# Performance work log

Measured on AMD Instinct MI355X. Metric: run time of the kernel, lower is better.

Reference implementation:

```python
import jax, jax.numpy as jnp
import numpy as np

TEMPERATURE = 0.07
EPS = 1e-8  # torch CosineSimilarity norm clamp

N, D, NUM_CLASSES = 4096, 768, 128


def setup_inputs() -> dict:
    key = jax.random.key(0)
    k1, k2, k3 = jax.random.split(key, 3)
    img_emb = jax.random.normal(k1, (N, D), dtype=jnp.float32)
    text_emb = jax.random.normal(k2, (N, D), dtype=jnp.float32)
    labels = jax.random.randint(k3, (N,), 0, NUM_CLASSES, dtype=jnp.int64)
    return {"img_emb": img_emb, "text_emb": text_emb, "labels": labels}


def reference(img_emb, text_emb, labels):
    # cosine similarity via normalize + matmul (avoids O(N^2 D) broadcast)
    img_n = img_emb / jnp.maximum(jnp.linalg.norm(img_emb, axis=-1, keepdims=True), EPS)
    txt_n = text_emb / jnp.maximum(jnp.linalg.norm(text_emb, axis=-1, keepdims=True), EPS)
    logits = jnp.einsum('id,jd->ij', img_n, txt_n) / TEMPERATURE  # [N, N]

    pos_mask = (labels[:, None] == labels[None, :]).astype(logits.dtype)  # [N, N]

    img2text = -(pos_mask * jax.nn.log_softmax(logits, axis=1)).sum(1).mean()
    text2img = -(pos_mask * jax.nn.log_softmax(logits, axis=0)).sum(0).mean()
    return (img2text + text2img) / 2
```

## Files before the change

kernel.cpp:

```cpp
#include <hip/hip_runtime.h>
#include <hip/hip_bf16.h>

#define N_ 4096
#define D_ 768
#define NCLS 128
#define BM 128
#define BN 128
#define BK 32
#define NSTEP 24

typedef __bf16 bf16x8 __attribute__((ext_vector_type(8)));
typedef float f32x4 __attribute__((ext_vector_type(4)));
typedef short s16x8 __attribute__((ext_vector_type(8)));

__global__ __launch_bounds__(256) void normalize_kernel(
    const float* __restrict__ img, const float* __restrict__ txt,
    __hip_bfloat16* __restrict__ img_nb, __hip_bfloat16* __restrict__ txt_nb,
    double* __restrict__ accs, unsigned* __restrict__ cnt) {
  if (blockIdx.x == 0 && threadIdx.x == 0) {
    accs[0] = 0.0;
    accs[1] = 0.0;
    *cnt = 0u;
  }
  int idx = blockIdx.x * 4 + (threadIdx.x >> 6);
  int lane = threadIdx.x & 63;
  const float* s;
  __hip_bfloat16* d;
  if (idx < N_) {
    s = img + (size_t)idx * D_;
    d = img_nb + (size_t)idx * D_;
  } else {
    s = txt + (size_t)(idx - N_) * D_;
    d = txt_nb + (size_t)(idx - N_) * D_;
  }
  float4 v0 = ((const float4*)s)[lane];
  float4 v1 = ((const float4*)s)[lane + 64];
  float4 v2 = ((const float4*)s)[lane + 128];
  float ss = v0.x * v0.x + v0.y * v0.y + v0.z * v0.z + v0.w * v0.w +
             v1.x * v1.x + v1.y * v1.y + v1.z * v1.z + v1.w * v1.w +
             v2.x * v2.x + v2.y * v2.y + v2.z * v2.z + v2.w * v2.w;
#pragma unroll
  for (int m = 32; m; m >>= 1) ss += __shfl_xor(ss, m);
  float inv = 1.0f / fmaxf(sqrtf(ss), 1e-8f);
  ushort4 o0, o1, o2;
  o0.x = __bfloat16_as_ushort(__float2bfloat16(v0.x * inv));
  o0.y = __bfloat16_as_ushort(__float2bfloat16(v0.y * inv));
  o0.z = __bfloat16_as_ushort(__float2bfloat16(v0.z * inv));
  o0.w = __bfloat16_as_ushort(__float2bfloat16(v0.w * inv));
  o1.x = __bfloat16_as_ushort(__float2bfloat16(v1.x * inv));
  o1.y = __bfloat16_as_ushort(__float2bfloat16(v1.y * inv));
  o1.z = __bfloat16_as_ushort(__float2bfloat16(v1.z * inv));
  o1.w = __bfloat16_as_ushort(__float2bfloat16(v1.w * inv));
  o2.x = __bfloat16_as_ushort(__float2bfloat16(v2.x * inv));
  o2.y = __bfloat16_as_ushort(__float2bfloat16(v2.y * inv));
  o2.z = __bfloat16_as_ushort(__float2bfloat16(v2.z * inv));
  o2.w = __bfloat16_as_ushort(__float2bfloat16(v2.w * inv));
  ((ushort4*)d)[lane] = o0;
  ((ushort4*)d)[lane + 64] = o1;
  ((ushort4*)d)[lane + 128] = o2;
}

__global__ __launch_bounds__(256) void gemm_epi_kernel(
    const unsigned short* __restrict__ A, const unsigned short* __restrict__ B,
    const int* __restrict__ labels, float* __restrict__ row_part,
    float* __restrict__ col_part, float* __restrict__ S_part) {
  __shared__ __align__(16) unsigned short As[2][4096];
  __shared__ __align__(16) unsigned short Bs[2][4096];
  __shared__ int labR[BM], labC[BN];
  __shared__ float rbuf[2][BM], cbuf[2][BN];
  __shared__ float sbuf[4];

  const int lin = blockIdx.y * 32 + blockIdx.x;
  const int xcd = lin & 7, idx = lin >> 3;
  const int bx = xcd * 4 + (idx & 3), by = idx >> 2;

  const int tid = threadIdx.x;
  const int lane = tid & 63, wave = tid >> 6;
  const int wr = wave >> 1, wc = wave & 1;
  const int g = lane >> 4, fr = lane & 15;
  const int rowBase = by * BM, colBase = bx * BN;

  if (tid < BM) labR[tid] = labels[rowBase + tid];
  else labC[tid - BM] = labels[colBase + tid - BM];

  const int gq = tid & 3, rbase = tid >> 2;
  const unsigned short* pa = A + (size_t)(rowBase + rbase) * D_ + gq * 8;
  const unsigned short* pb = B + (size_t)(colBase + rbase) * D_ + gq * 8;
  const int wpos = (rbase * 4 + (gq ^ ((rbase >> 1) & 3))) * 8;

  f32x4 acc[4][4] = {};

  const int sw = (g ^ ((fr >> 1) & 3)) * 8;

  s16x8 ra[2], rb[2];
#pragma unroll
  for (int j = 0; j < 2; ++j) {
    ra[j] = *(const s16x8*)(pa + (size_t)(64 * j) * D_);
    rb[j] = *(const s16x8*)(pb + (size_t)(64 * j) * D_);
  }
#pragma unroll
  for (int j = 0; j < 2; ++j) {
    *(s16x8*)&As[0][wpos + j * 2048] = ra[j];
    *(s16x8*)&Bs[0][wpos + j * 2048] = rb[j];
  }
#pragma unroll
  for (int j = 0; j < 2; ++j) {
    ra[j] = *(const s16x8*)(pa + (size_t)(64 * j) * D_ + BK);
    rb[j] = *(const s16x8*)(pb + (size_t)(64 * j) * D_ + BK);
  }
  __syncthreads();

  for (int u = 0; u < NSTEP; ++u) {
    const unsigned short* as_ = As[u & 1];
    const unsigned short* bs_ = Bs[u & 1];
    bf16x8 af[4], bf[4];
#pragma unroll
    for (int m = 0; m < 4; ++m)
      af[m] = *(const bf16x8*)&as_[(wr * 64 + m * 16 + fr) * 32 + sw];
#pragma unroll
    for (int n = 0; n < 4; ++n)
      bf[n] = *(const bf16x8*)&bs_[(wc * 64 + n * 16 + fr) * 32 + sw];
    if (u + 1 < NSTEP) {
      unsigned short* aw = As[(u + 1) & 1];
      unsigned short* bw = Bs[(u + 1) & 1];
#pragma unroll
      for (int j = 0; j < 2; ++j) {
        *(s16x8*)&aw[wpos + j * 2048] = ra[j];
        *(s16x8*)&bw[wpos + j * 2048] = rb[j];
      }
    }
#pragma unroll
    for (int m = 0; m < 4; ++m)
#pragma unroll
      for (int n = 0; n < 4; ++n)
        acc[m][n] = __builtin_amdgcn_mfma_f32_16x16x32_bf16(af[m], bf[n], acc[m][n], 0, 0, 0);
    if (u + 2 < NSTEP) {
      const int k0 = (u + 2) * BK;
#pragma unroll
      for (int j = 0; j < 2; ++j) {
        ra[j] = *(const s16x8*)(pa + (size_t)(64 * j) * D_ + k0);
        rb[j] = *(const s16x8*)(pb + (size_t)(64 * j) * D_ + k0);
      }
    }
    __syncthreads();
  }

  const float scale = 14.285714285714286f;
  float sPart = 0.f;
  float colAcc[4] = {0.f, 0.f, 0.f, 0.f};
#pragma unroll
  for (int m = 0; m < 4; ++m) {
    float ra2[4] = {0.f, 0.f, 0.f, 0.f};
#pragma unroll
    for (int n = 0; n < 4; ++n) {
      int col = wc * 64 + n * 16 + fr;
      int lc = labC[col];
#pragma unroll
      for (int r = 0; r < 4; ++r) {
        float v = acc[m][n][r] * scale;
        float e = __expf(v);
        ra2[r] += e;
        colAcc[n] += e;
        int row = wr * 64 + m * 16 + g * 4 + r;
        if (labR[row] == lc) sPart += v;
      }
    }
#pragma unroll
    for (int r = 0; r < 4; ++r) {
      float x = ra2[r];
      x += __shfl_xor(x, 1);
      x += __shfl_xor(x, 2);
      x += __shfl_xor(x, 4);
      x += __shfl_xor(x, 8);
      if (fr == 0) rbuf[wc][wr * 64 + m * 16 + g * 4 + r] = x;
    }
  }
#pragma unroll
  for (int n = 0; n < 4; ++n) {
    float x = colAcc[n];
    x += __shfl_xor(x, 16);
    x += __shfl_xor(x, 32);
    if (g == 0) cbuf[wr][wc * 64 + n * 16 + fr] = x;
  }
  float s = sPart;
#pragma unroll
  for (int m = 32; m; m >>= 1) s += __shfl_xor(s, m);
  if (lane == 0) sbuf[wave] = s;
  __syncthreads();
  if (tid < BM)
    row_part[(size_t)bx * N_ + rowBase + tid] = rbuf[0][tid] + rbuf[1][tid];
  else
    col_part[(size_t)by * N_ + colBase + (tid - BM)] = cbuf[0][tid - BM] + cbuf[1][tid - BM];
  if (tid == 0) S_part[by * 32 + bx] = sbuf[0] + sbuf[1] + sbuf[2] + sbuf[3];
}

__global__ __launch_bounds__(256) void reduce_kernel(
    const float* __restrict__ row_part, const float* __restrict__ col_part,
    const float* __restrict__ S_part, const int* __restrict__ labels,
    double* __restrict__ accs, unsigned* __restrict__ cnt, float* __restrict__ out) {
  __shared__ int hist[NCLS];
  int tid = threadIdx.x;
  if (tid < NCLS) hist[tid] = 0;
  __syncthreads();
  for (int j = tid; j < N_; j += 256) atomicAdd(&hist[labels[j]], 1);
  __syncthreads();

  int i = blockIdx.x * 256 + tid;
  float rs = 0.f, cs = 0.f;
#pragma unroll
  for (int b = 0; b < 32; ++b) {
    rs += row_part[(size_t)b * N_ + i];
    cs += col_part[(size_t)b * N_ + i];
  }
  int c = hist[labels[i]];
  double term = (double)c * ((double)logf(rs) + (double)logf(cs));
  double sterm = (i < 1024) ? (double)S_part[i] : 0.0;
#pragma unroll
  for (int m = 32; m; m >>= 1) {
    term += __shfl_xor(term, m);
    sterm += __shfl_xor(sterm, m);
  }
  __shared__ double tbuf[4], sb[4];
  int lane = tid & 63, w = tid >> 6;
  if (lane == 0) { tbuf[w] = term; sb[w] = sterm; }
  __syncthreads();
  if (tid == 0) {
    atomicAdd(&accs[0], tbuf[0] + tbuf[1] + tbuf[2] + tbuf[3]);
    atomicAdd(&accs[1], sb[0] + sb[1] + sb[2] + sb[3]);
    __threadfence();
    unsigned old = atomicAdd(cnt, 1u);
    if (old == 15u) {
      double t = atomicAdd(&accs[0], 0.0);
      double s2 = atomicAdd(&accs[1], 0.0);
      out[0] = (float)((t - 2.0 * s2) / (2.0 * (double)N_));
    }
  }
}

extern "C" void kernel_launch(void* const* d_in, const int* in_sizes, int n_in,
                              void* d_out, int out_size, void* d_ws, size_t ws_size,
                              hipStream_t stream) {
  const float* img = (const float*)d_in[0];
  const float* txt = (const float*)d_in[1];
  const int* labels = (const int*)d_in[2];
  float* out = (float*)d_out;
  char* ws = (char*)d_ws;

  __hip_bfloat16* img_nb = (__hip_bfloat16*)(ws);
  __hip_bfloat16* txt_nb = (__hip_bfloat16*)(ws + 6291456);
  float* row_part = (float*)(ws + 12582912);
  float* col_part = (float*)(ws + 13107200);
  float* S_part = (float*)(ws + 13631488);
  double* accs = (double*)(ws + 13635584);
  unsigned* cnt = (unsigned*)(ws + 13635600);

  normalize_kernel<<<2 * N_ / 4, 256, 0, stream>>>(img, txt, img_nb, txt_nb, accs, cnt);
  gemm_epi_kernel<<<dim3(32, 32), 256, 0, stream>>>(
      (const unsigned short*)img_nb, (const unsigned short*)txt_nb, labels,
      row_part, col_part, S_part);
  reduce_kernel<<<16, 256, 0, stream>>>(row_part, col_part, S_part, labels, accs, cnt, out);
}
```

Baseline: 56.29 us.

## Write normalized embeddings in MFMA fragment layout and load operands directly from global

The normalize kernel now writes the bf16 embeddings in a pre-tiled layout that matches the 16x16x32 MFMA fragment order, with 16-row groups and 8-element k chunks. The GEMM then drops the LDS double buffer, its swizzle and the per-step barriers, and each wave loads its A/B fragments straight from global memory as contiguous 16-byte vectors. This removes LDS traffic and synchronization. In exchange, fragments shared across waves are re-read through the cache instead of being shared via LDS, and there is no explicit prefetch, so load latency may be exposed.

```diff
diff --git a/kernel.cpp b/kernel.cpp
--- a/kernel.cpp
+++ b/kernel.cpp
@@ -6,16 +6,15 @@
 #define NCLS 128
 #define BM 128
 #define BN 128
-#define BK 32
+#define NG 96
 #define NSTEP 24
 
 typedef __bf16 bf16x8 __attribute__((ext_vector_type(8)));
 typedef float f32x4 __attribute__((ext_vector_type(4)));
-typedef short s16x8 __attribute__((ext_vector_type(8)));
 
 __global__ __launch_bounds__(256) void normalize_kernel(
     const float* __restrict__ img, const float* __restrict__ txt,
-    __hip_bfloat16* __restrict__ img_nb, __hip_bfloat16* __restrict__ txt_nb,
+    unsigned short* __restrict__ img_f, unsigned short* __restrict__ txt_f,
     double* __restrict__ accs, unsigned* __restrict__ cnt) {
   if (blockIdx.x == 0 && threadIdx.x == 0) {
     accs[0] = 0.0;
@@ -25,13 +24,14 @@
   int idx = blockIdx.x * 4 + (threadIdx.x >> 6);
   int lane = threadIdx.x & 63;
   const float* s;
-  __hip_bfloat16* d;
+  unsigned short* d;
   if (idx < N_) {
     s = img + (size_t)idx * D_;
-    d = img_nb + (size_t)idx * D_;
+    d = img_f;
   } else {
     s = txt + (size_t)(idx - N_) * D_;
-    d = txt_nb + (size_t)(idx - N_) * D_;
+    d = txt_f;
+    idx -= N_;
   }
   float4 v0 = ((const float4*)s)[lane];
   float4 v1 = ((const float4*)s)[lane + 64];
@@ -42,30 +42,24 @@
 #pragma unroll
   for (int m = 32; m; m >>= 1) ss += __shfl_xor(ss, m);
   float inv = 1.0f / fmaxf(sqrtf(ss), 1e-8f);
-  ushort4 o0, o1, o2;
-  o0.x = __bfloat16_as_ushort(__float2bfloat16(v0.x * inv));
-  o0.y = __bfloat16_as_ushort(__float2bfloat16(v0.y * inv));
-  o0.z = __bfloat16_as_ushort(__float2bfloat16(v0.z * inv));
-  o0.w = __bfloat16_as_ushort(__float2bfloat16(v0.w * inv));
-  o1.x = __bfloat16_as_ushort(__float2bfloat16(v1.x * inv));
-  o1.y = __bfloat16_as_ushort(__float2bfloat16(v1.y * inv));
-  o1.z = __bfloat16_as_ushort(__float2bfloat16(v1.z * inv));
-  o1.w = __bfloat16_as_ushort(__float2bfloat16(v1.w * inv));
-  o2.x = __bfloat16_as_ushort(__float2bfloat16(v2.x * inv));
-  o2.y = __bfloat16_as_ushort(__float2bfloat16(v2.y * inv));
-  o2.z = __bfloat16_as_ushort(__float2bfloat16(v2.z * inv));
-  o2.w = __bfloat16_as_ushort(__float2bfloat16(v2.w * inv));
-  ((ushort4*)d)[lane] = o0;
-  ((ushort4*)d)[lane + 64] = o1;
-  ((ushort4*)d)[lane + 128] = o2;
+  const int tb = (idx >> 4) * NG, fo = (idx & 15) * 8;
+#pragma unroll
+  for (int p = 0; p < 3; ++p) {
+    float4 v = (p == 0) ? v0 : (p == 1) ? v1 : v2;
+    int k = 4 * lane + p * 256;
+    ushort4 o;
+    o.x = __bfloat16_as_ushort(__float2bfloat16(v.x * inv));
+    o.y = __bfloat16_as_ushort(__float2bfloat16(v.y * inv));
+    o.z = __bfloat16_as_ushort(__float2bfloat16(v.z * inv));
+    o.w = __bfloat16_as_ushort(__float2bfloat16(v.w * inv));
+    *(ushort4*)&d[(size_t)(tb + (k >> 3)) * 128 + fo + (k & 7)] = o;
+  }
 }
 
 __global__ __launch_bounds__(256) void gemm_epi_kernel(
-    const unsigned short* __restrict__ A, const unsigned short* __restrict__ B,
+    const unsigned short* __restrict__ Af, const unsigned short* __restrict__ Bf,
     const int* __restrict__ labels, float* __restrict__ row_part,
     float* __restrict__ col_part, float* __restrict__ S_part) {
-  __shared__ __align__(16) unsigned short As[2][4096];
-  __shared__ __align__(16) unsigned short Bs[2][4096];
   __shared__ int labR[BM], labC[BN];
   __shared__ float rbuf[2][BM], cbuf[2][BN];
   __shared__ float sbuf[4];
@@ -83,67 +77,31 @@
   if (tid < BM) labR[tid] = labels[rowBase + tid];
   else labC[tid - BM] = labels[colBase + tid - BM];
 
-  const int gq = tid & 3, rbase = tid >> 2;
-  const unsigned short* pa = A + (size_t)(rowBase + rbase) * D_ + gq * 8;
-  const unsigned short* pb = B + (size_t)(colBase + rbase) * D_ + gq * 8;
-  const int wpos = (rbase * 4 + (gq ^ ((rbase >> 1) & 3))) * 8;
+  const unsigned short* pa[4];
+  const unsigned short* pb[4];
+#pragma unroll
+  for (int m = 0; m < 4; ++m)
+    pa[m] = Af + (size_t)((by * 8 + wr * 4 + m) * NG + g) * 128 + fr * 8;
+#pragma unroll
+  for (int n = 0; n < 4; ++n)
+    pb[n] = Bf + (size_t)((bx * 8 + wc * 4 + n) * NG + g) * 128 + fr * 8;
 
   f32x4 acc[4][4] = {};
 
-  const int sw = (g ^ ((fr >> 1) & 3)) * 8;
-
-  s16x8 ra[2], rb[2];
-#pragma unroll
-  for (int j = 0; j < 2; ++j) {
-    ra[j] = *(const s16x8*)(pa + (size_t)(64 * j) * D_);
-    rb[j] = *(const s16x8*)(pb + (size_t)(64 * j) * D_);
-  }
-#pragma unroll
-  for (int j = 0; j < 2; ++j) {
-    *(s16x8*)&As[0][wpos + j * 2048] = ra[j];
-    *(s16x8*)&Bs[0][wpos + j * 2048] = rb[j];
-  }
-#pragma unroll
-  for (int j = 0; j < 2; ++j) {
-    ra[j] = *(const s16x8*)(pa + (size_t)(64 * j) * D_ + BK);
-    rb[j] = *(const s16x8*)(pb + (size_t)(64 * j) * D_ + BK);
-  }
-  __syncthreads();
-
   for (int u = 0; u < NSTEP; ++u) {
-    const unsigned short* as_ = As[u & 1];
-    const unsigned short* bs_ = Bs[u & 1];
+    const int off = u * 512;
     bf16x8 af[4], bf[4];
 #pragma unroll
-    for (int m = 0; m < 4; ++m)
-      af[m] = *(const bf16x8*)&as_[(wr * 64 + m * 16 + fr) * 32 + sw];
-#pragma unroll
-    for (int n = 0; n < 4; ++n)
-      bf[n] = *(const bf16x8*)&bs_[(wc * 64 + n * 16 + fr) * 32 + sw];
-    if (u + 1 < NSTEP) {
-      unsigned short* aw = As[(u + 1) & 1];
-      unsigned short* bw = Bs[(u + 1) & 1];
-#pragma unroll
-      for (int j = 0; j < 2; ++j) {
-        *(s16x8*)&aw[wpos + j * 2048] = ra[j];
-        *(s16x8*)&bw[wpos + j * 2048] = rb[j];
-      }
-    }
+    for (int m = 0; m < 4; ++m) af[m] = *(const bf16x8*)(pa[m] + off);
+#pragma unroll
+    for (int n = 0; n < 4; ++n) bf[n] = *(const bf16x8*)(pb[n] + off);
 #pragma unroll
     for (int m = 0; m < 4; ++m)
 #pragma unroll
       for (int n = 0; n < 4; ++n)
         acc[m][n] = __builtin_amdgcn_mfma_f32_16x16x32_bf16(af[m], bf[n], acc[m][n], 0, 0, 0);
-    if (u + 2 < NSTEP) {
-      const int k0 = (u + 2) * BK;
-#pragma unroll
-      for (int j = 0; j < 2; ++j) {
-        ra[j] = *(const s16x8*)(pa + (size_t)(64 * j) * D_ + k0);
-        rb[j] = *(const s16x8*)(pb + (size_t)(64 * j) * D_ + k0);
-      }
-    }
-    __syncthreads();
-  }
+  }
+  __syncthreads();
 
   const float scale = 14.285714285714286f;
   float sPart = 0.f;
@@ -246,17 +204,16 @@
   float* out = (float*)d_out;
   char* ws = (char*)d_ws;
 
-  __hip_bfloat16* img_nb = (__hip_bfloat16*)(ws);
-  __hip_bfloat16* txt_nb = (__hip_bfloat16*)(ws + 6291456);
+  unsigned short* img_f = (unsigned short*)(ws);
+  unsigned short* txt_f = (unsigned short*)(ws + 6291456);
   float* row_part = (float*)(ws + 12582912);
   float* col_part = (float*)(ws + 13107200);
   float* S_part = (float*)(ws + 13631488);
   double* accs = (double*)(ws + 13635584);
   unsigned* cnt = (unsigned*)(ws + 13635600);
 
-  normalize_kernel<<<2 * N_ / 4, 256, 0, stream>>>(img, txt, img_nb, txt_nb, accs, cnt);
+  normalize_kernel<<<2 * N_ / 4, 256, 0, stream>>>(img, txt, img_f, txt_f, accs, cnt);
   gemm_epi_kernel<<<dim3(32, 32), 256, 0, stream>>>(
-      (const unsigned short*)img_nb, (const unsigned short*)txt_nb, labels,
-      row_part, col_part, S_part);
+      img_f, txt_f, labels, row_part, col_part, S_part);
   reduce_kernel<<<16, 256, 0, stream>>>(row_part, col_part, S_part, labels, accs, cnt, out);
 }
```

After: 97.16 us. 72.6% more time.
